# Kernel optimization log

Measured on AMD Instinct MI355X. Metric: run time of the kernel, lower is better.

## Reference

```python
import jax, jax.numpy as jnp
import numpy as np

# Architecture constants (match init_kwargs)
SHAPES = [(128, 128), (64, 64), (32, 32), (16, 16)]  # (H, W) per level
L, P, NH, D, DH = 4, 4, 8, 256, 32
NLAYERS, DFFN, BS = 6, 1024, 2
N = sum(h * w for h, w in SHAPES)  # 21760


def setup_inputs() -> dict:
    key = jax.random.key(0)
    ks = iter(jax.random.split(key, 64))
    def nrm(shape, s=0.02):
        return s * jax.random.normal(next(ks), shape, jnp.float32)
    inp = {}
    for i, (h, w) in enumerate(SHAPES):
        inp[f"src{i}"] = jax.random.normal(next(ks), (BS, D, h, w), jnp.float32)
        inp[f"pos{i}"] = 0.1 * jax.random.normal(next(ks), (BS, D, h, w), jnp.float32)
    inp["level_embed"] = nrm((L, D), 1.0)
    inp["W_off"] = nrm((NLAYERS, NH * L * P * 2, D)); inp["b_off"] = nrm((NLAYERS, NH * L * P * 2), 0.5)
    inp["W_attn"] = nrm((NLAYERS, NH * L * P, D)); inp["b_attn"] = jnp.zeros((NLAYERS, NH * L * P), jnp.float32)
    inp["W_val"] = nrm((NLAYERS, D, D)); inp["b_val"] = jnp.zeros((NLAYERS, D), jnp.float32)
    inp["W_out"] = nrm((NLAYERS, D, D)); inp["b_out"] = jnp.zeros((NLAYERS, D), jnp.float32)
    inp["g_na"] = jnp.ones((NLAYERS, D), jnp.float32); inp["g_nf"] = jnp.ones((NLAYERS, D), jnp.float32)
    inp["ls_a"] = jnp.full((NLAYERS, D), 1e-4, jnp.float32); inp["ls_f"] = jnp.full((NLAYERS, D), 1e-4, jnp.float32)
    inp["W1"] = nrm((NLAYERS, DFFN, D)); inp["b1"] = jnp.zeros((NLAYERS, DFFN), jnp.float32)
    inp["W3"] = nrm((NLAYERS, DFFN, D)); inp["b3"] = jnp.zeros((NLAYERS, DFFN), jnp.float32)
    inp["W2"] = nrm((NLAYERS, D, DFFN)); inp["b2"] = jnp.zeros((NLAYERS, D), jnp.float32)
    return inp


def rmsnorm(x, g):
    return x * jax.lax.rsqrt(jnp.mean(x * x, axis=-1, keepdims=True) + 1e-6) * g


def reference_points():
    # valid_ratios == 1 (all shapes divisible by 32 -> masks all False), so
    # reference points are identical across levels: [N, 2] in (x, y) normalized.
    refs = []
    for h, w in SHAPES:
        ry = (jnp.arange(h, dtype=jnp.float32) + 0.5) / h
        rx = (jnp.arange(w, dtype=jnp.float32) + 0.5) / w
        gy, gx = jnp.meshgrid(ry, rx, indexing='ij')
        refs.append(jnp.stack([gx.ravel(), gy.ravel()], axis=-1))
    return jnp.concatenate(refs, axis=0)


def deform_sample(value, loc, aw):
    # value: [bs, N, NH, DH]; loc: [bs, Nq, NH, L, P, 2]; aw: [bs, Nq, NH, L, P]
    bs, nq = loc.shape[0], loc.shape[1]
    out = jnp.zeros((bs, NH, nq, DH), jnp.float32)
    start = 0
    for l, (Hl, Wl) in enumerate(SHAPES):
        val = value[:, start:start + Hl * Wl].transpose(0, 2, 1, 3)  # [bs,NH,HW,DH]
        start += Hl * Wl
        # grid_sample(align_corners=False): pixel = loc * size - 0.5, zero padding
        x = loc[:, :, :, l, :, 0] * Wl - 0.5  # [bs,Nq,NH,P]
        y = loc[:, :, :, l, :, 1] * Hl - 0.5
        x0 = jnp.floor(x); y0 = jnp.floor(y)
        acc = jnp.zeros((bs, NH, nq, P, DH), jnp.float32)
        for dx in (0.0, 1.0):
            for dy in (0.0, 1.0):
                xi = x0 + dx; yi = y0 + dy
                w = (1.0 - jnp.abs(x - xi)) * (1.0 - jnp.abs(y - yi))
                valid = (xi >= 0) & (xi < Wl) & (yi >= 0) & (yi < Hl)
                idx = (jnp.clip(yi, 0, Hl - 1) * Wl + jnp.clip(xi, 0, Wl - 1)).astype(jnp.int32)
                idx = idx.transpose(0, 2, 1, 3).reshape(bs, NH, nq * P)
                g = jnp.take_along_axis(val, idx[..., None], axis=2).reshape(bs, NH, nq, P, DH)
                acc = acc + g * (w * valid).transpose(0, 2, 1, 3)[..., None]
        out = out + (acc * aw[:, :, :, l].transpose(0, 2, 1, 3)[..., None]).sum(axis=3)
    return out.transpose(0, 2, 1, 3).reshape(bs, nq, NH * DH)


def msda(q, qpos, ref, Wo, bo, Wa, ba, Wv, bv, Wp, bp):
    # q: pre-normed tokens used both as query and value (identity disabled)
    bs, nq, _ = q.shape
    qin = q + qpos
    value = (q @ Wv.T + bv).reshape(bs, nq, NH, DH)
    off = (qin @ Wo.T + bo).reshape(bs, nq, NH, L, P, 2)
    aw = jax.nn.softmax((qin @ Wa.T + ba).reshape(bs, nq, NH, L * P), axis=-1)
    aw = aw.reshape(bs, nq, NH, L, P)
    normalizer = jnp.array([[w, h] for h, w in SHAPES], jnp.float32)  # [L,2] (x=W,y=H)
    loc = ref[None, :, None, None, None, :] + off / normalizer[None, None, None, :, None, :]
    samp = deform_sample(value, loc, aw)
    return samp @ Wp.T + bp


def reference(src0, src1, src2, src3, pos0, pos1, pos2, pos3, level_embed,
              W_off, b_off, W_attn, b_attn, W_val, b_val, W_out, b_out,
              g_na, g_nf, ls_a, ls_f, W1, b1, W3, b3, W2, b2):
    srcs = [src0, src1, src2, src3]
    poss = [pos0, pos1, pos2, pos3]
    q = jnp.concatenate([s.reshape(BS, D, -1).transpose(0, 2, 1) for s in srcs], axis=1)
    posf = jnp.concatenate(
        [p.reshape(BS, D, -1).transpose(0, 2, 1) + level_embed[i] for i, p in enumerate(poss)], axis=1)
    ref = reference_points()
    for i in range(NLAYERS):
        n = rmsnorm(q, g_na[i])
        a = msda(n, posf, ref, W_off[i], b_off[i], W_attn[i], b_attn[i],
                 W_val[i], b_val[i], W_out[i], b_out[i])
        q = q + ls_a[i] * a
        n = rmsnorm(q, g_nf[i])
        f = (jax.nn.silu(n @ W1[i].T + b1[i]) * (n @ W3[i].T + b3[i])) @ W2[i].T + b2[i]
        q = q + ls_f[i] * f
    spatial_shapes = jnp.array(SHAPES, jnp.int32)
    level_start_index = jnp.concatenate(
        [jnp.zeros((1,), jnp.int32), jnp.cumsum(spatial_shapes.prod(1))[:-1]])
    return q, spatial_shapes, level_start_index
```

## Files before the change

### kernel.cpp

```cpp
#include <hip/hip_runtime.h>

typedef unsigned short u16;
typedef unsigned int   u32;
typedef __bf16 bf16x8 __attribute__((ext_vector_type(8)));
typedef float  f32x4  __attribute__((ext_vector_type(4)));
typedef u16    u16x4  __attribute__((ext_vector_type(4)));
typedef u32    u32x4  __attribute__((ext_vector_type(4)));

#define NTOK 21760
#define TTOK 43520
#define DMODEL 256

__device__ __forceinline__ u16 f2bf(float f){
  u32 u = __builtin_bit_cast(u32, f);
  u32 r = u + 0x7fffu + ((u >> 16) & 1u);
  return (u16)(r >> 16);
}
__device__ __forceinline__ float bf2f(u16 h){
  u32 u = ((u32)h) << 16;
  return __builtin_bit_cast(float, u);
}
__device__ __forceinline__ float lo16(u32 u){ return __builtin_bit_cast(float, u << 16); }
__device__ __forceinline__ float hi16(u32 u){ return __builtin_bit_cast(float, u & 0xffff0000u); }

__device__ __forceinline__ void gld16(const u16* g, u16* l){
  __builtin_amdgcn_global_load_lds((const __attribute__((address_space(1))) void*)g,
                                   (__attribute__((address_space(3))) void*)l, 16, 0, 0);
}

__global__ void cvt_plain(const float* __restrict__ s, u16* __restrict__ d, int n){
  int i = blockIdx.x * 256 + threadIdx.x;
  if (i < n) d[i] = f2bf(s[i]);
}
__global__ void build_oa_w(const float* __restrict__ Wo, const float* __restrict__ Wa, u16* __restrict__ dst){
  int i = blockIdx.x * 256 + threadIdx.x;
  if (i >= 6*384*256) return;
  int l = i / (384*256); int rem = i % (384*256); int r = rem >> 8; int c = rem & 255;
  float v = (r < 256) ? Wo[((size_t)l*256 + r)*256 + c] : Wa[((size_t)l*128 + (r-256))*256 + c];
  dst[i] = f2bf(v);
}
__global__ void build_oa_b(const float* __restrict__ bo, const float* __restrict__ ba, float* __restrict__ dst){
  int i = blockIdx.x * 256 + threadIdx.x;
  if (i >= 6*384) return;
  int l = i / 384; int r = i % 384;
  dst[i] = (r < 256) ? bo[l*256 + r] : ba[l*128 + (r-256)];
}
__global__ void build_w13(const float* __restrict__ W1, const float* __restrict__ W3, u16* __restrict__ dst){
  int i = blockIdx.x * 256 + threadIdx.x;
  if (i >= 6*2048*256) return;
  int l = i / (2048*256); int rem = i % (2048*256); int r = rem >> 8; int c = rem & 255;
  int f = r >> 1; int s = r & 1;
  const float* W = s ? W3 : W1;
  dst[i] = f2bf(W[((size_t)l*1024 + f)*256 + c]);
}
__global__ void build_b13(const float* __restrict__ b1, const float* __restrict__ b3, float* __restrict__ dst){
  int i = blockIdx.x * 256 + threadIdx.x;
  if (i >= 6*2048) return;
  int l = i / 2048; int r = i % 2048;
  dst[i] = (r & 1) ? b3[l*1024 + (r>>1)] : b1[l*1024 + (r>>1)];
}

__global__ __launch_bounds__(256)
void prep_level(const float* __restrict__ src, const float* __restrict__ pos,
                const float* __restrict__ lemb, float* __restrict__ q,
                u16* __restrict__ posf, int HW, int nstart){
  __shared__ float tS[32][65];
  __shared__ float tP[32][65];
  int b  = blockIdx.z;
  int d0 = blockIdx.y * 32;
  int n0 = blockIdx.x * 64;
  int tx = threadIdx.x & 63, ty = threadIdx.x >> 6;
  #pragma unroll
  for (int i = 0; i < 8; ++i){
    int d = i*4 + ty;
    size_t gi = ((size_t)b*DMODEL + d0 + d) * HW + n0 + tx;
    tS[d][tx] = src[gi];
    tP[d][tx] = pos[gi];
  }
  __syncthreads();
  int dc = threadIdx.x & 31, nl0 = threadIdx.x >> 5;
  float le = lemb[d0 + dc];
  #pragma unroll
  for (int ii = 0; ii < 8; ++ii){
    int nl = nl0 + ii*8;
    size_t oi = ((size_t)b*NTOK + nstart + n0 + nl) * DMODEL + d0 + dc;
    q[oi]    = tS[dc][nl];
    posf[oi] = f2bf(tP[dc][nl] + le);
  }
}

__global__ void tail_writer(float* __restrict__ out){
  const float vals[12] = {128.f,128.f,64.f,64.f,32.f,32.f,16.f,16.f,
                          0.f,16384.f,20480.f,21504.f};
  int t = threadIdx.x;
  if (t < 12) out[(size_t)TTOK*DMODEL + t] = vals[t];
}

__global__ __launch_bounds__(256)
void rmsnorm_k(const float* __restrict__ q, const float* __restrict__ g,
               const u16* __restrict__ posf, u16* __restrict__ nout,
               u16* __restrict__ qinout){
  int tok  = blockIdx.x*4 + (threadIdx.x >> 6);
  int lane = threadIdx.x & 63;
  const f32x4* qr = (const f32x4*)(q + (size_t)tok*DMODEL);
  f32x4 v = qr[lane];
  float ss = v[0]*v[0] + v[1]*v[1] + v[2]*v[2] + v[3]*v[3];
  #pragma unroll
  for (int o = 32; o > 0; o >>= 1) ss += __shfl_xor(ss, o);
  float sc = rsqrtf(ss * (1.0f/256.0f) + 1e-6f);
  f32x4 gv = ((const f32x4*)g)[lane];
  float nf[4]; u16x4 nv;
  #pragma unroll
  for (int r = 0; r < 4; ++r){ nf[r] = v[r]*sc*gv[r]; nv[r] = f2bf(nf[r]); }
  ((u16x4*)(nout + (size_t)tok*DMODEL))[lane] = nv;
  if (qinout){
    u16x4 pf = ((const u16x4*)(posf + (size_t)tok*DMODEL))[lane];
    u16x4 qv;
    #pragma unroll
    for (int r = 0; r < 4; ++r) qv[r] = f2bf(nf[r] + bf2f(pf[r]));
    ((u16x4*)(qinout + (size_t)tok*DMODEL))[lane] = qv;
  }
}

template<int EPI>
__global__ __launch_bounds__(256)
void gemm_bt(const u16* __restrict__ A, const u16* __restrict__ B,
             const float* __restrict__ bias, void* __restrict__ outp,
             const float* __restrict__ ls, int K, int ldo){
  __shared__ u16 lds[2][2][4096];
  const int tid = threadIdx.x, lane = tid & 63, w = tid >> 6;
  const int wm = w >> 1, wn = w & 1;

  const int gx = gridDim.x;
  const int nwg = gx * gridDim.y;
  const int id  = blockIdx.y * gx + blockIdx.x;
  const int q8 = nwg >> 3, r8 = nwg & 7;
  const int xcd = id & 7, pos = id >> 3;
  const int nid = (xcd < r8 ? xcd * (q8 + 1) : r8 * (q8 + 1) + (xcd - r8) * q8) + pos;
  const int bn = (nid % gx) * 128, bm = (nid / gx) * 128;

  const int fr = lane & 15, ks = lane >> 4;

  const u16* gA = A + (size_t)(bm + w*32 + (lane >> 2)) * K + (lane & 3) * 8;
  const u16* gB = B + (size_t)(bn + w*32 + (lane >> 2)) * K + (lane & 3) * 8;
  const size_t rstep = (size_t)16 * K;

  f32x4 acc[4][4];
  #pragma unroll
  for (int m = 0; m < 4; ++m)
    #pragma unroll
    for (int n = 0; n < 4; ++n) acc[m][n] = (f32x4){0.f,0.f,0.f,0.f};

  const int aoff = (wm*64 + fr)*32 + ks*8;
  const int boff = (wn*64 + fr)*32 + ks*8;

  auto STAGE = [&](int buf, int k0){
    gld16(gA + k0,         &lds[buf][0][w*1024]);
    gld16(gA + k0 + rstep, &lds[buf][0][w*1024 + 512]);
    gld16(gB + k0,         &lds[buf][1][w*1024]);
    gld16(gB + k0 + rstep, &lds[buf][1][w*1024 + 512]);
  };

  const int nk = K >> 5;
  STAGE(0, 0);
  __syncthreads();
  int buf = 0;
  for (int t = 0; t < nk; ++t){
    if (t + 1 < nk) STAGE(buf ^ 1, (t + 1) * 32);
    bf16x8 af[4], bb[4];
    #pragma unroll
    for (int m = 0; m < 4; ++m) af[m] = *(const bf16x8*)&lds[buf][0][aoff + m*512];
    #pragma unroll
    for (int n = 0; n < 4; ++n) bb[n] = *(const bf16x8*)&lds[buf][1][boff + n*512];
    #pragma unroll
    for (int m = 0; m < 4; ++m)
      #pragma unroll
      for (int n = 0; n < 4; ++n)
        acc[m][n] = __builtin_amdgcn_mfma_f32_16x16x32_bf16(af[m], bb[n], acc[m][n], 0, 0, 0);
    __syncthreads();
    buf ^= 1;
  }

  const int colb = bn + wn*64 + fr;
  const int rowb = bm + wm*64 + ks*4;

  if (EPI == 0){
    u16* o = (u16*)outp;
    #pragma unroll
    for (int n = 0; n < 4; ++n){
      int col = colb + n*16; float bv = bias[col];
      #pragma unroll
      for (int m = 0; m < 4; ++m){
        int row = rowb + m*16;
        #pragma unroll
        for (int r = 0; r < 4; ++r)
          o[(size_t)(row + r)*ldo + col] = f2bf(acc[m][n][r] + bv);
      }
    }
  } else if (EPI == 1){
    u16* o = (u16*)outp;
    #pragma unroll
    for (int n = 0; n < 4; ++n){
      int col = colb + n*16; float bv = bias[col];
      int f = col >> 1; bool even = ((col & 1) == 0);
      #pragma unroll
      for (int m = 0; m < 4; ++m){
        int row = rowb + m*16;
        #pragma unroll
        for (int r = 0; r < 4; ++r){
          float v = acc[m][n][r] + bv;
          float other = __shfl_xor(v, 1);
          if (even){
            float res = (v / (1.0f + __expf(-v))) * other;
            o[(size_t)(row + r)*ldo + f] = f2bf(res);
          }
        }
      }
    }
  } else {
    float* o = (float*)outp;
    #pragma unroll
    for (int n = 0; n < 4; ++n){
      int col = colb + n*16; float bv = bias[col]; float lv = ls[col];
      #pragma unroll
      for (int m = 0; m < 4; ++m){
        int row = rowb + m*16;
        #pragma unroll
        for (int r = 0; r < 4; ++r){
          size_t ix = (size_t)(row + r)*ldo + col;
          o[ix] += lv * (acc[m][n][r] + bv);
        }
      }
    }
  }
}

__global__ __launch_bounds__(256)
void sampler_k(const u16* __restrict__ oa, const u16* __restrict__ value,
               u16* __restrict__ samp){
  int nid = (blockIdx.x & 7) * 340 + (blockIdx.x >> 3);
  int t = nid * 256 + threadIdx.x;
  int half = t & 1;
  int pair = t >> 1;
  int head = pair & 7;
  int q = (pair >> 3) % NTOK;
  int b = pair / (NTOK * 8);

  int st, lw, sh;
  if (q < 16384){ st = 0;     lw = 128; sh = 7; }
  else if (q < 20480){ st = 16384; lw = 64; sh = 6; }
  else if (q < 21504){ st = 20480; lw = 32; sh = 5; }
  else { st = 21504; lw = 16; sh = 4; }
  int loc = q - st;
  int j = loc & (lw - 1), i = loc >> sh;
  float invW = 1.0f / (float)lw;
  float rx = (j + 0.5f) * invW, ry = (i + 0.5f) * invW;

  const u16* oq = oa + (size_t)(b*NTOK + q) * 384;
  float lg[8];
  const u32* lg32 = (const u32*)(oq + 256 + head*16) + half*4;
  #pragma unroll
  for (int p = 0; p < 4; ++p){ u32 wd = lg32[p]; lg[2*p] = lo16(wd); lg[2*p+1] = hi16(wd); }
  float mx = -1e30f;
  #pragma unroll
  for (int p = 0; p < 8; ++p) mx = fmaxf(mx, lg[p]);
  mx = fmaxf(mx, __shfl_xor(mx, 1));
  float ssum = 0.f;
  #pragma unroll
  for (int p = 0; p < 8; ++p){ lg[p] = __expf(lg[p] - mx); ssum += lg[p]; }
  ssum += __shfl_xor(ssum, 1);
  float inv = 1.0f / ssum;

  float acc[32];
  #pragma unroll
  for (int d = 0; d < 32; ++d) acc[d] = 0.f;

  const u32* op32 = (const u32*)(oq + head*32);
  #pragma unroll
  for (int il = 0; il < 2; ++il){
    const int l = half*2 + il;
    const int Wl    = il ? (half ? 16 : 64)    : (half ? 32 : 128);
    const int start = il ? (half ? 21504 : 16384) : (half ? 20480 : 0);
    #pragma unroll
    for (int p = 0; p < 4; ++p){
      u32 wd = op32[l*4 + p];
      float x = rx * Wl + lo16(wd) - 0.5f;
      float y = ry * Wl + hi16(wd) - 0.5f;
      float x0f = floorf(x), y0f = floorf(y);
      int x0 = (int)x0f, y0 = (int)y0f;
      float fx = x - x0f, fy = y - y0f;
      float wp = lg[il*4 + p];
      #pragma unroll
      for (int c = 0; c < 4; ++c){
        int xi = x0 + (c & 1), yi = y0 + (c >> 1);
        float wc = ((c & 1) ? fx : 1.f - fx) * ((c >> 1) ? fy : 1.f - fy) * wp;
        if (xi >= 0 && xi < Wl && yi >= 0 && yi < Wl && wc != 0.f){
          const u32x4* vp = (const u32x4*)(value +
              ((size_t)(b*NTOK + start + yi*Wl + xi) * DMODEL + head*32));
          #pragma unroll
          for (int u4 = 0; u4 < 4; ++u4){
            u32x4 vv = vp[u4];
            #pragma unroll
            for (int jj = 0; jj < 4; ++jj){
              acc[8*u4 + 2*jj]     += wc * lo16(vv[jj]);
              acc[8*u4 + 2*jj + 1] += wc * hi16(vv[jj]);
            }
          }
        }
      }
    }
  }

  #pragma unroll
  for (int d = 0; d < 32; ++d) acc[d] += __shfl_xor(acc[d], 1);

  u16* out = samp + (size_t)(b*NTOK + q) * DMODEL + head*32 + half*16;
  #pragma unroll
  for (int d = 0; d < 16; d += 4){
    u16x4 o4;
    #pragma unroll
    for (int r = 0; r < 4; ++r) o4[r] = f2bf(acc[half*16 + d + r] * inv);
    *(u16x4*)(out + d) = o4;
  }
}

extern "C" void kernel_launch(void* const* d_in, const int* in_sizes, int n_in,
                              void* d_out, int out_size, void* d_ws, size_t ws_size,
                              hipStream_t stream){
  const float* src[4] = {(const float*)d_in[0], (const float*)d_in[2],
                         (const float*)d_in[4], (const float*)d_in[6]};
  const float* pos[4] = {(const float*)d_in[1], (const float*)d_in[3],
                         (const float*)d_in[5], (const float*)d_in[7]};
  const float* le     = (const float*)d_in[8];
  const float* W_off  = (const float*)d_in[9];  const float* b_off  = (const float*)d_in[10];
  const float* W_attn = (const float*)d_in[11]; const float* b_attn = (const float*)d_in[12];
  const float* W_val  = (const float*)d_in[13]; const float* b_val  = (const float*)d_in[14];
  const float* W_out  = (const float*)d_in[15]; const float* b_out  = (const float*)d_in[16];
  const float* g_na   = (const float*)d_in[17]; const float* g_nf   = (const float*)d_in[18];
  const float* ls_a   = (const float*)d_in[19]; const float* ls_f   = (const float*)d_in[20];
  const float* W1     = (const float*)d_in[21]; const float* b1     = (const float*)d_in[22];
  const float* W3     = (const float*)d_in[23]; const float* b3     = (const float*)d_in[24];
  const float* W2     = (const float*)d_in[25]; const float* b2     = (const float*)d_in[26];

  char* ws = (char*)d_ws;
  u16*   wv   = (u16*)  (ws + 0);
  u16*   wpj  = (u16*)  (ws + 786432);
  u16*   w2b  = (u16*)  (ws + 1572864);
  u16*   woa  = (u16*)  (ws + 4718592);
  float* boa  = (float*)(ws + 5898240);
  u16*   w13  = (u16*)  (ws + 5907456);
  float* bi13 = (float*)(ws + 12198912);
  u16*   posfb= (u16*)  (ws + 12248064);
  u16*   nb   = (u16*)  (ws + 34530304);
  u16*   qinb = (u16*)  (ws + 56812544);
  u16*   valb = (u16*)  (ws + 79094784);
  u16*   oab  = (u16*)  (ws + 101377024);
  u16*   sampb= (u16*)  (ws + 134800384);
  u16*   hb   = qinb;
  float* qf   = (float*)d_out;

  cvt_plain<<<(393216+255)/256, 256, 0, stream>>>(W_val, wv, 393216);
  cvt_plain<<<(393216+255)/256, 256, 0, stream>>>(W_out, wpj, 393216);
  cvt_plain<<<(1572864+255)/256, 256, 0, stream>>>(W2, w2b, 1572864);
  build_oa_w<<<(589824+255)/256, 256, 0, stream>>>(W_off, W_attn, woa);
  build_oa_b<<<(2304+255)/256, 256, 0, stream>>>(b_off, b_attn, boa);
  build_w13<<<(3145728+255)/256, 256, 0, stream>>>(W1, W3, w13);
  build_b13<<<(12288+255)/256, 256, 0, stream>>>(b1, b3, bi13);

  const int HW[4]  = {16384, 4096, 1024, 256};
  const int nst[4] = {0, 16384, 20480, 21504};
  for (int l = 0; l < 4; ++l){
    dim3 g(HW[l]/64, 8, 2);
    prep_level<<<g, 256, 0, stream>>>(src[l], pos[l], le + l*256, qf, posfb, HW[l], nst[l]);
  }
  tail_writer<<<1, 64, 0, stream>>>(qf);

  for (int l = 0; l < 6; ++l){
    rmsnorm_k<<<10880, 256, 0, stream>>>(qf, g_na + l*256, posfb, nb, qinb);
    gemm_bt<0><<<dim3(3,340), 256, 0, stream>>>(qinb, woa + (size_t)l*98304, boa + l*384, oab, nullptr, 256, 384);
    gemm_bt<0><<<dim3(2,340), 256, 0, stream>>>(nb, wv + (size_t)l*65536, b_val + l*256, valb, nullptr, 256, 256);
    sampler_k<<<2720, 256, 0, stream>>>(oab, valb, sampb);
    gemm_bt<2><<<dim3(2,340), 256, 0, stream>>>(sampb, wpj + (size_t)l*65536, b_out + l*256, qf, ls_a + l*256, 256, 256);
    rmsnorm_k<<<10880, 256, 0, stream>>>(qf, g_nf + l*256, nullptr, nb, nullptr);
    gemm_bt<1><<<dim3(16,340), 256, 0, stream>>>(nb, w13 + (size_t)l*524288, bi13 + l*2048, hb, nullptr, 256, 1024);
    gemm_bt<2><<<dim3(2,340), 256, 0, stream>>>(hb, w2b + (size_t)l*262144, b2 + l*256, qf, ls_f + l*256, 1024, 256);
  }
  (void)in_sizes; (void)n_in; (void)out_size; (void)ws_size;
}
```

Baseline: 2.311 ms.

## Store value and offset/attn tensors head-major so sampler gathers from per-head planes

```diff
diff --git a/kernel.cpp b/kernel.cpp
--- a/kernel.cpp
+++ b/kernel.cpp
@@ -217,7 +217,7 @@
         }
       }
     }
-  } else {
+  } else if (EPI == 2){
     float* o = (float*)outp;
     #pragma unroll
     for (int n = 0; n < 4; ++n){
@@ -232,19 +232,55 @@
         }
       }
     }
+  } else if (EPI == 3){
+    u16* o = (u16*)outp;
+    #pragma unroll
+    for (int n = 0; n < 4; ++n){
+      int col = colb + n*16; float bv = bias[col];
+      int head = col >> 5, ch = col & 31;
+      #pragma unroll
+      for (int m = 0; m < 4; ++m){
+        int row = rowb + m*16;
+        #pragma unroll
+        for (int r = 0; r < 4; ++r){
+          int rw = row + r;
+          int bb2 = rw >= NTOK ? 1 : 0;
+          int tok = rw - bb2 * NTOK;
+          o[((size_t)(bb2*8 + head)*NTOK + tok)*32 + ch] = f2bf(acc[m][n][r] + bv);
+        }
+      }
+    }
+  } else {
+    u16* o = (u16*)outp;
+    #pragma unroll
+    for (int n = 0; n < 4; ++n){
+      int col = colb + n*16; float bv = bias[col];
+      int head, within;
+      if (col < 256){ head = col >> 5; within = col & 31; }
+      else { int c = col - 256; head = c >> 4; within = 32 + (c & 15); }
+      #pragma unroll
+      for (int m = 0; m < 4; ++m){
+        int row = rowb + m*16;
+        #pragma unroll
+        for (int r = 0; r < 4; ++r){
+          int rw = row + r;
+          int bb2 = rw >= NTOK ? 1 : 0;
+          int tok = rw - bb2 * NTOK;
+          o[((size_t)(bb2*8 + head)*NTOK + tok)*48 + within] = f2bf(acc[m][n][r] + bv);
+        }
+      }
+    }
   }
 }
 
 __global__ __launch_bounds__(256)
-void sampler_k(const u16* __restrict__ oa, const u16* __restrict__ value,
+void sampler_k(const u16* __restrict__ oa48, const u16* __restrict__ valpl,
                u16* __restrict__ samp){
   int nid = (blockIdx.x & 7) * 340 + (blockIdx.x >> 3);
-  int t = nid * 256 + threadIdx.x;
-  int half = t & 1;
-  int pair = t >> 1;
-  int head = pair & 7;
-  int q = (pair >> 3) % NTOK;
-  int b = pair / (NTOK * 8);
+  int bh = nid / 170, qb = nid % 170;
+  int lane = threadIdx.x & 63, wv = threadIdx.x >> 6;
+  int half = lane >> 5;
+  int q = qb * 128 + wv * 32 + (lane & 31);
 
   int st, lw, sh;
   if (q < 16384){ st = 0;     lw = 128; sh = 7; }
@@ -256,34 +292,34 @@
   float invW = 1.0f / (float)lw;
   float rx = (j + 0.5f) * invW, ry = (i + 0.5f) * invW;
 
-  const u16* oq = oa + (size_t)(b*NTOK + q) * 384;
+  const u16* oq = oa48 + ((size_t)bh * NTOK + q) * 48;
   float lg[8];
-  const u32* lg32 = (const u32*)(oq + 256 + head*16) + half*4;
+  const u32* lg32 = (const u32*)(oq + 32) + half * 4;
   #pragma unroll
   for (int p = 0; p < 4; ++p){ u32 wd = lg32[p]; lg[2*p] = lo16(wd); lg[2*p+1] = hi16(wd); }
   float mx = -1e30f;
   #pragma unroll
   for (int p = 0; p < 8; ++p) mx = fmaxf(mx, lg[p]);
-  mx = fmaxf(mx, __shfl_xor(mx, 1));
+  mx = fmaxf(mx, __shfl_xor(mx, 32));
   float ssum = 0.f;
   #pragma unroll
   for (int p = 0; p < 8; ++p){ lg[p] = __expf(lg[p] - mx); ssum += lg[p]; }
-  ssum += __shfl_xor(ssum, 1);
+  ssum += __shfl_xor(ssum, 32);
   float inv = 1.0f / ssum;
 
   float acc[32];
   #pragma unroll
   for (int d = 0; d < 32; ++d) acc[d] = 0.f;
 
-  const u32* op32 = (const u32*)(oq + head*32);
+  const u32* op32 = (const u32*)oq + half * 8;
+  const u16* plane = valpl + (size_t)bh * NTOK * 32;
   #pragma unroll
   for (int il = 0; il < 2; ++il){
-    const int l = half*2 + il;
-    const int Wl    = il ? (half ? 16 : 64)    : (half ? 32 : 128);
-    const int start = il ? (half ? 21504 : 16384) : (half ? 20480 : 0);
+    const int Wl    = half ? (il ? 16 : 32)    : (il ? 64 : 128);
+    const int start = half ? (il ? 21504 : 20480) : (il ? 16384 : 0);
     #pragma unroll
     for (int p = 0; p < 4; ++p){
-      u32 wd = op32[l*4 + p];
+      u32 wd = op32[il*4 + p];
       float x = rx * Wl + lo16(wd) - 0.5f;
       float y = ry * Wl + hi16(wd) - 0.5f;
       float x0f = floorf(x), y0f = floorf(y);
@@ -295,8 +331,7 @@
         int xi = x0 + (c & 1), yi = y0 + (c >> 1);
         float wc = ((c & 1) ? fx : 1.f - fx) * ((c >> 1) ? fy : 1.f - fy) * wp;
         if (xi >= 0 && xi < Wl && yi >= 0 && yi < Wl && wc != 0.f){
-          const u32x4* vp = (const u32x4*)(value +
-              ((size_t)(b*NTOK + start + yi*Wl + xi) * DMODEL + head*32));
+          const u32x4* vp = (const u32x4*)(plane + (size_t)(start + yi*Wl + xi) * 32);
           #pragma unroll
           for (int u4 = 0; u4 < 4; ++u4){
             u32x4 vv = vp[u4];
@@ -312,9 +347,9 @@
   }
 
   #pragma unroll
-  for (int d = 0; d < 32; ++d) acc[d] += __shfl_xor(acc[d], 1);
-
-  u16* out = samp + (size_t)(b*NTOK + q) * DMODEL + head*32 + half*16;
+  for (int d = 0; d < 32; ++d) acc[d] += __shfl_xor(acc[d], 32);
+
+  u16* out = samp + ((size_t)(bh >> 3) * NTOK + q) * DMODEL + (bh & 7) * 32 + half * 16;
   #pragma unroll
   for (int d = 0; d < 16; d += 4){
     u16x4 o4;
@@ -377,8 +412,8 @@
 
   for (int l = 0; l < 6; ++l){
     rmsnorm_k<<<10880, 256, 0, stream>>>(qf, g_na + l*256, posfb, nb, qinb);
-    gemm_bt<0><<<dim3(3,340), 256, 0, stream>>>(qinb, woa + (size_t)l*98304, boa + l*384, oab, nullptr, 256, 384);
-    gemm_bt<0><<<dim3(2,340), 256, 0, stream>>>(nb, wv + (size_t)l*65536, b_val + l*256, valb, nullptr, 256, 256);
+    gemm_bt<4><<<dim3(3,340), 256, 0, stream>>>(qinb, woa + (size_t)l*98304, boa + l*384, oab, nullptr, 256, 384);
+    gemm_bt<3><<<dim3(2,340), 256, 0, stream>>>(nb, wv + (size_t)l*65536, b_val + l*256, valb, nullptr, 256, 256);
     sampler_k<<<2720, 256, 0, stream>>>(oab, valb, sampb);
     gemm_bt<2><<<dim3(2,340), 256, 0, stream>>>(sampb, wpj + (size_t)l*65536, b_out + l*256, qf, ls_a + l*256, 256, 256);
     rmsnorm_k<<<10880, 256, 0, stream>>>(qf, g_nf + l*256, nullptr, nb, nullptr);
```

Measured after the change: 2.227 ms. 1.04x faster.
